# Kernel optimization log

Measured on AMD Instinct MI355X. Metric: run time of the kernel, lower is better.

The kernel has to match this reference:

```python
import jax, jax.numpy as jnp
import numpy as np

NEG_SLOPE = 0.2
BN_EPS = 1e-5


def _gat_conv(x, src, dst, W, a_src, a_dst, b, n_nodes):
    # PyG GATConv, heads=1: linear, per-edge leaky-relu score, per-dst softmax, scatter-add.
    h = x @ W  # [N, C]
    e = jax.nn.leaky_relu((h @ a_src)[src] + (h @ a_dst)[dst], NEG_SLOPE)  # [E]
    m = jax.ops.segment_max(e, dst, num_segments=n_nodes)
    m = jnp.where(jnp.isfinite(m), m, 0.0)  # nodes with no in-edges
    w = jnp.exp(e - m[dst])
    denom = jax.ops.segment_sum(w, dst, num_segments=n_nodes)
    alpha = w / (denom[dst] + 1e-16)  # [E]
    out = jax.ops.segment_sum(alpha[:, None] * h[src], dst, num_segments=n_nodes)
    return out + b


def setup_inputs() -> dict:
    key = jax.random.key(0)
    N, E, Q, C = 50000, 800000, 200000, 128
    ks = jax.random.split(key, 12)
    sc = 1.0 / np.sqrt(C)
    d = {
        "embedding": jax.random.normal(ks[0], (N, C), jnp.float32) * 0.1,
        "W1": jax.random.normal(ks[1], (C, C), jnp.float32) * sc,
        "a_src1": jax.random.normal(ks[2], (C,), jnp.float32) * sc,
        "a_dst1": jax.random.normal(ks[3], (C,), jnp.float32) * sc,
        "b1": jnp.zeros((C,), jnp.float32),
        "gamma": jnp.ones((C,), jnp.float32),
        "beta": jnp.zeros((C,), jnp.float32),
        "rmean": jnp.zeros((C,), jnp.float32),
        "rvar": jnp.ones((C,), jnp.float32),
        "W2": jax.random.normal(ks[4], (C, C), jnp.float32) * sc,
        "a_src2": jax.random.normal(ks[5], (C,), jnp.float32) * sc,
        "a_dst2": jax.random.normal(ks[6], (C,), jnp.float32) * sc,
        "b2": jnp.zeros((C,), jnp.float32),
        "Wp1": jax.random.normal(ks[7], (C, C), jnp.float32) * sc,
        "bp1": jnp.zeros((C,), jnp.float32),
        "Wp2": jax.random.normal(ks[8], (C, 1), jnp.float32) * sc,
        "bp2": jnp.zeros((1,), jnp.float32),
        "edge_index": jax.random.randint(ks[9], (2, E), 0, N, jnp.int32),
        "edges": jax.random.randint(ks[10], (2, Q), 0, N, jnp.int32),
    }
    return d


def reference(embedding, W1, a_src1, a_dst1, b1, gamma, beta, rmean, rvar,
              W2, a_src2, a_dst2, b2, Wp1, bp1, Wp2, bp2, edge_index, edges):
    N = embedding.shape[0]
    src, dst = edge_index[0], edge_index[1]
    # conv0 -> BN (eval, running stats) -> ReLU (dropout inactive in eval)
    x = _gat_conv(embedding, src, dst, W1, a_src1, a_dst1, b1, N)
    x = (x - rmean) * jax.lax.rsqrt(rvar + BN_EPS) * gamma + beta
    x = jax.nn.relu(x)
    # final conv
    x = _gat_conv(x, src, dst, W2, a_src2, a_dst2, b2, N)
    # LinkPredictor: elementwise product of endpoint embeddings -> MLP -> sigmoid
    h = x[edges[0]] * x[edges[1]]  # [Q, C]
    h = jax.nn.relu(h @ Wp1 + bp1)
    out = jax.nn.sigmoid(h @ Wp2 + bp2)
    return out[:, 0]
```

## Files before the change

### kernel.cpp

```cpp
#include <hip/hip_runtime.h>
#include <hip/hip_bf16.h>
#include <math.h>
#include <stdint.h>
#include <string.h>

#define NEG_SLOPE 0.2f
#define BN_EPS 1e-5f

typedef __attribute__((ext_vector_type(8))) short short8;
typedef __attribute__((ext_vector_type(4))) float float4v;

static __device__ __forceinline__ unsigned short f2bf(float f) {
    union { float f; unsigned u; } v; v.f = f;
    unsigned r = (v.u + 0x7fffu + ((v.u >> 16) & 1u)) >> 16;
    return (unsigned short)r;
}
static __device__ __forceinline__ float bf2f(unsigned short u) {
    union { unsigned u; float f; } v; v.u = ((unsigned)u) << 16;
    return v.f;
}

#define BK_CAP 8192
#define BK_EPB 4096
#define LP_RS 136

__global__ __launch_bounds__(256) void zero_init(int* __restrict__ p, int n) {
    int i = threadIdx.x + blockIdx.x * 256;
    if (i < n) p[i] = 0;
}

static __device__ __forceinline__ void scatter_body(
    int* lcnt, int* lbase, int blk,
    const int* __restrict__ src, const int* __restrict__ dst,
    int* __restrict__ bcur, unsigned int* __restrict__ bucket, int E) {
    int t = threadIdx.x;
    int e0 = blk * BK_EPB;
    lcnt[t] = 0;
    __syncthreads();

    int es[16], ed[16];
#pragma unroll
    for (int u = 0; u < 16; ++u) {
        int i = e0 + u * 256 + t;
        if (i < E) {
            es[u] = src[i];
            ed[u] = dst[i];
            atomicAdd(&lcnt[ed[u] >> 8], 1);
        } else {
            ed[u] = -1;
        }
    }
    __syncthreads();
    int c = lcnt[t];
    if (c > 0) lbase[t] = atomicAdd(&bcur[t], c);
    __syncthreads();
    lcnt[t] = 0;
    __syncthreads();
#pragma unroll
    for (int u = 0; u < 16; ++u) {
        if (ed[u] >= 0) {
            int bin = ed[u] >> 8;
            int r = atomicAdd(&lcnt[bin], 1);
            int slot = lbase[bin] + r;
            if (slot < BK_CAP)
                bucket[(size_t)bin * BK_CAP + slot] =
                    ((unsigned)(ed[u] & 255) << 24) | (unsigned)es[u];
        }
    }
}

__global__ __launch_bounds__(256) void prep_scatter(
    const float* __restrict__ W1, const float* __restrict__ W2,
    const float* __restrict__ Wp1,
    unsigned short* __restrict__ wt1, unsigned short* __restrict__ wt2,
    unsigned short* __restrict__ wtp,
    const float* __restrict__ gamma, const float* __restrict__ beta,
    const float* __restrict__ rmean, const float* __restrict__ rvar,
    float* __restrict__ bnsc, float* __restrict__ bnsh,
    const int* __restrict__ src, const int* __restrict__ dst,
    int* __restrict__ bcur, unsigned int* __restrict__ bucket, int E) {
    __shared__ int lcnt[256];
    __shared__ int lbase[256];
    int b = blockIdx.x;
    if (b < 192) {
        const float* W = (b < 64) ? W1 : (b < 128) ? W2 : Wp1;
        unsigned short* WT = (b < 64) ? wt1 : (b < 128) ? wt2 : wtp;
        int idx = (b & 63) * 256 + threadIdx.x;
        int k = idx >> 7, n = idx & 127;
        WT[n * 128 + k] = f2bf(W[idx]);
    } else if (b == 192) {
        if (threadIdx.x < 128) {
            int c = threadIdx.x;
            float s = gamma[c] * rsqrtf(rvar[c] + BN_EPS);
            bnsc[c] = s;
            bnsh[c] = beta[c] - rmean[c] * s;
        }
    } else {
        scatter_body(lcnt, lbase, b - 193, src, dst, bcur, bucket, E);
    }
}

static __device__ __forceinline__ void fill_body(
    char* base, int b,
    const int* __restrict__ bcur, const unsigned int* __restrict__ bucket,
    int* __restrict__ gcnt,
    int* __restrict__ offs, int* __restrict__ ends,
    int* __restrict__ csr, int N) {
    unsigned int* rec = (unsigned int*)base;
    int* cnt = (int*)(base + BK_CAP * 4);
    int* sc  = cnt + 256;
    int* pb  = sc + 256;
    int t = threadIdx.x;
    const unsigned int* gb = &bucket[(size_t)b * BK_CAP];
    cnt[t] = 0;
    int c = bcur[b];
    if (c < 0) c = 0;
    if (c > BK_CAP) c = BK_CAP;
    if (t == 0) *pb = atomicAdd(gcnt, c);
    for (int i = t; i < c; i += 256) rec[i] = gb[i];
    __syncthreads();
    for (int i = t; i < c; i += 256) atomicAdd(&cnt[rec[i] >> 24], 1);
    __syncthreads();
    int v = cnt[t];
    sc[t] = v;
    __syncthreads();
    for (int d = 1; d < 256; d <<= 1) {
        int u = (t >= d) ? sc[t - d] : 0;
        __syncthreads();
        sc[t] += u;
        __syncthreads();
    }
    int myoff = *pb + sc[t] - v;
    int node = (b << 8) + t;
    if (node < N) {
        offs[node] = myoff;
        ends[node] = myoff + v;
    }
    cnt[t] = myoff;
    __syncthreads();
    for (int i = t; i < c; i += 256) {
        unsigned int rv = rec[i];
        int r = atomicAdd(&cnt[rv >> 24], 1);
        csr[r] = (int)(rv & 0xffffffu);
    }
}

template <bool BF16_IN>
static __device__ __forceinline__ void gemm_body(
    unsigned short* sA, unsigned short* sW, int bid,
    const void* __restrict__ Xv,
    const unsigned short* __restrict__ WT,
    const float* __restrict__ a_src, const float* __restrict__ a_dst,
    unsigned short* __restrict__ H,
    float* __restrict__ s_src, float* __restrict__ s_dst, int N)
{
    const float* Xf = (const float*)Xv;
    const unsigned short* Xh = (const unsigned short*)Xv;
    int tid = threadIdx.x;
    int r0 = bid * 128;

#pragma unroll
    for (int it = 0; it < 8; ++it) {
        int idx = it * 2048 + tid * 8;
        int n = idx >> 7, k = idx & 127;
        *(short8*)&sW[n * LP_RS + k] = *(const short8*)&WT[idx];
    }
#pragma unroll
    for (int it = 0; it < 16; ++it) {
        int r = it * 8 + (tid >> 5);
        int c = (tid & 31) * 4;
        int row = r0 + r;
        ushort4 u = make_ushort4(0, 0, 0, 0);
        if (row < N) {
            if (BF16_IN) {
                u = *(const ushort4*)&Xh[(size_t)row * 128 + c];
            } else {
                float4 x = *(const float4*)&Xf[(size_t)row * 128 + c];
                u.x = f2bf(x.x); u.y = f2bf(x.y); u.z = f2bf(x.z); u.w = f2bf(x.w);
            }
        }
        *(ushort4*)&sA[r * LP_RS + c] = u;
    }
    __syncthreads();

    int wave = tid >> 6, lane = tid & 63;
    int ln = lane & 15, quad = lane >> 4;
    int rowbase = wave * 32;

    short8 af[2][4];
#pragma unroll
    for (int m = 0; m < 2; ++m)
#pragma unroll
        for (int kt = 0; kt < 4; ++kt)
            af[m][kt] = *(const short8*)&sA[(rowbase + m * 16 + ln) * LP_RS + kt * 32 + quad * 8];

    float4v acc[2][8];
#pragma unroll
    for (int m = 0; m < 2; ++m)
#pragma unroll
        for (int n = 0; n < 8; ++n)
            acc[m][n] = float4v{0.f, 0.f, 0.f, 0.f};

#pragma unroll
    for (int n = 0; n < 8; ++n) {
#pragma unroll
        for (int kt = 0; kt < 4; ++kt) {
            short8 bf = *(const short8*)&sW[(n * 16 + ln) * LP_RS + kt * 32 + quad * 8];
            acc[0][n] = __builtin_amdgcn_mfma_f32_16x16x32_bf16(af[0][kt], bf, acc[0][n], 0, 0, 0);
            acc[1][n] = __builtin_amdgcn_mfma_f32_16x16x32_bf16(af[1][kt], bf, acc[1][n], 0, 0, 0);
        }
    }

    float asr[8], adr[8];
#pragma unroll
    for (int n = 0; n < 8; ++n) {
        asr[n] = a_src[n * 16 + ln];
        adr[n] = a_dst[n * 16 + ln];
    }
#pragma unroll
    for (int m = 0; m < 2; ++m) {
        int rb = r0 + rowbase + m * 16 + quad * 4;
#pragma unroll
        for (int n = 0; n < 8; ++n) {
            int col = n * 16 + ln;
            float4v a = acc[m][n];
            if (rb + 0 < N) H[(size_t)(rb + 0) * 128 + col] = f2bf(a[0]);
            if (rb + 1 < N) H[(size_t)(rb + 1) * 128 + col] = f2bf(a[1]);
            if (rb + 2 < N) H[(size_t)(rb + 2) * 128 + col] = f2bf(a[2]);
            if (rb + 3 < N) H[(size_t)(rb + 3) * 128 + col] = f2bf(a[3]);
        }
#pragma unroll
        for (int r = 0; r < 4; ++r) {
            float ps = 0.f, pd = 0.f;
#pragma unroll
            for (int n = 0; n < 8; ++n) {
                float v = acc[m][n][r];
                ps = fmaf(v, asr[n], ps);
                pd = fmaf(v, adr[n], pd);
            }
#pragma unroll
            for (int o = 1; o < 16; o <<= 1) {
                ps += __shfl_xor(ps, o);
                pd += __shfl_xor(pd, o);
            }
            int row = rb + r;
            if (ln == 0 && row < N) { s_src[row] = ps; s_dst[row] = pd; }
        }
    }
}

__global__ __launch_bounds__(256) void gemm1_fill(
    const void* __restrict__ Xv, const unsigned short* __restrict__ WT,
    const float* __restrict__ a_src, const float* __restrict__ a_dst,
    unsigned short* __restrict__ H, float* __restrict__ s_src,
    float* __restrict__ s_dst, int N, int gblk,
    const int* __restrict__ bcur, const unsigned int* __restrict__ bucket,
    int* __restrict__ gcnt, int* __restrict__ offs, int* __restrict__ ends,
    int* __restrict__ csr) {
    __shared__ uint4 smem[4352];
    int b = blockIdx.x;
    if (b < gblk) {
        unsigned short* sA = (unsigned short*)smem;
        gemm_body<false>(sA, sA + 128 * LP_RS, b, Xv, WT, a_src, a_dst,
                         H, s_src, s_dst, N);
    } else {
        fill_body((char*)smem, b - gblk, bcur, bucket, gcnt, offs, ends, csr, N);
    }
}

template <bool BF16_IN>
__global__ __launch_bounds__(256) void gemm_mfma(
    const void* __restrict__ Xv, const unsigned short* __restrict__ WT,
    const float* __restrict__ a_src, const float* __restrict__ a_dst,
    unsigned short* __restrict__ H, float* __restrict__ s_src,
    float* __restrict__ s_dst, int N) {
    __shared__ uint4 smem[4352];
    unsigned short* sA = (unsigned short*)smem;
    gemm_body<BF16_IN>(sA, sA + 128 * LP_RS, blockIdx.x, Xv, WT, a_src, a_dst,
                       H, s_src, s_dst, N);
}

__global__ __launch_bounds__(256) void gat_gather(const unsigned short* __restrict__ H,
                                                  const int* __restrict__ offs,
                                                  const int* __restrict__ ends,
                                                  const int* __restrict__ csr,
                                                  const float* __restrict__ s_src,
                                                  const float* __restrict__ s_dst,
                                                  const float* __restrict__ bias,
                                                  const float* __restrict__ bn_scale,
                                                  const float* __restrict__ bn_shift,
                                                  int do_bn_relu,
                                                  unsigned short* __restrict__ out, int N) {
    int wave = threadIdx.x >> 6, lane = threadIdx.x & 63;
    int half = lane >> 5, hl = lane & 31;
    int node = blockIdx.x * 8 + wave * 2 + half;
    if (node >= N) return;
    int c0 = hl * 4;
    int beg = offs[node], end = ends[node];
    float sd = s_dst[node];

    float a0 = 0.f, a1 = 0.f, a2 = 0.f, a3 = 0.f;
    float sw = 0.f;
    for (int chunk = beg; chunk < end; chunk += 32) {
        int i = chunk + hl;
        int sidx = 0;
        float w = 0.f;
        if (i < end) {
            sidx = csr[i];
            float e = s_src[sidx] + sd;
            e = (e >= 0.f) ? e : NEG_SLOPE * e;
            w = expf(e);
        }
        sw += w;
        int cnt = end - chunk;
        if (cnt > 32) cnt = 32;
        int u = 0;
        for (; u + 8 <= cnt; u += 8) {
            int s[8]; float ww[8]; ushort4 hv[8];
#pragma unroll
            for (int j = 0; j < 8; ++j) {
                s[j]  = __shfl(sidx, u + j, 32);
                ww[j] = __shfl(w, u + j, 32);
            }
#pragma unroll
            for (int j = 0; j < 8; ++j)
                hv[j] = *(const ushort4*)&H[(size_t)s[j] * 128 + c0];
#pragma unroll
            for (int j = 0; j < 8; ++j) {
                a0 = fmaf(ww[j], bf2f(hv[j].x), a0);
                a1 = fmaf(ww[j], bf2f(hv[j].y), a1);
                a2 = fmaf(ww[j], bf2f(hv[j].z), a2);
                a3 = fmaf(ww[j], bf2f(hv[j].w), a3);
            }
        }
        for (; u + 4 <= cnt; u += 4) {
            int s[4]; float ww[4]; ushort4 hv[4];
#pragma unroll
            for (int j = 0; j < 4; ++j) {
                s[j]  = __shfl(sidx, u + j, 32);
                ww[j] = __shfl(w, u + j, 32);
            }
#pragma unroll
            for (int j = 0; j < 4; ++j)
                hv[j] = *(const ushort4*)&H[(size_t)s[j] * 128 + c0];
#pragma unroll
            for (int j = 0; j < 4; ++j) {
                a0 = fmaf(ww[j], bf2f(hv[j].x), a0);
                a1 = fmaf(ww[j], bf2f(hv[j].y), a1);
                a2 = fmaf(ww[j], bf2f(hv[j].z), a2);
                a3 = fmaf(ww[j], bf2f(hv[j].w), a3);
            }
        }
        for (; u < cnt; ++u) {
            int sj = __shfl(sidx, u, 32);
            float wj = __shfl(w, u, 32);
            ushort4 hv = *(const ushort4*)&H[(size_t)sj * 128 + c0];
            a0 = fmaf(wj, bf2f(hv.x), a0);
            a1 = fmaf(wj, bf2f(hv.y), a1);
            a2 = fmaf(wj, bf2f(hv.z), a2);
            a3 = fmaf(wj, bf2f(hv.w), a3);
        }
    }
#pragma unroll
    for (int o = 16; o; o >>= 1) sw += __shfl_xor(sw, o);
    float inv = 1.f / (sw + 1e-16f);

    float o0 = a0 * inv + bias[c0 + 0];
    float o1 = a1 * inv + bias[c0 + 1];
    float o2 = a2 * inv + bias[c0 + 2];
    float o3 = a3 * inv + bias[c0 + 3];
    if (do_bn_relu) {
        o0 = fmaxf(o0 * bn_scale[c0 + 0] + bn_shift[c0 + 0], 0.f);
        o1 = fmaxf(o1 * bn_scale[c0 + 1] + bn_shift[c0 + 1], 0.f);
        o2 = fmaxf(o2 * bn_scale[c0 + 2] + bn_shift[c0 + 2], 0.f);
        o3 = fmaxf(o3 * bn_scale[c0 + 3] + bn_shift[c0 + 3], 0.f);
    }
    ushort4 ov;
    ov.x = f2bf(o0); ov.y = f2bf(o1); ov.z = f2bf(o2); ov.w = f2bf(o3);
    *(ushort4*)&out[(size_t)node * 128 + c0] = ov;
}

__global__ __launch_bounds__(512) void link_pred_mfma(
    const unsigned short* __restrict__ X,
    const int* __restrict__ E0, const int* __restrict__ E1,
    const unsigned short* __restrict__ WTg,
    const float* __restrict__ bp1,
    const float* __restrict__ Wp2,
    const float* __restrict__ bp2_p,
    float* __restrict__ out, int Q)
{
    __shared__ unsigned short sW[128 * LP_RS];
    int tid = threadIdx.x;
    int wave = tid >> 6, lane = tid & 63;
    int ln = lane & 15, quad = lane >> 4;

    int tile = blockIdx.x * 8 + wave;
    int qbase = tile * 32;

    int ea[2], eb[2];
#pragma unroll
    for (int m = 0; m < 2; ++m) {
        int q = qbase + m * 16 + ln;
        if (q >= Q) q = Q - 1;
        ea[m] = E0[q];
        eb[m] = E1[q];
    }

#pragma unroll
    for (int it = 0; it < 4; ++it) {
        int idx = it * 4096 + tid * 8;
        int n = idx >> 7, k = idx & 127;
        *(short8*)&sW[n * LP_RS + k] = *(const short8*)&WTg[idx];
    }

    short8 ra[2][4], rb[2][4];
#pragma unroll
    for (int m = 0; m < 2; ++m) {
        const unsigned short* pa = &X[(size_t)ea[m] * 128 + quad * 8];
        const unsigned short* pb = &X[(size_t)eb[m] * 128 + quad * 8];
#pragma unroll
        for (int kt = 0; kt < 4; ++kt) {
            ra[m][kt] = *(const short8*)(pa + kt * 32);
            rb[m][kt] = *(const short8*)(pb + kt * 32);
        }
    }

    float bias[8], w2c[8];
#pragma unroll
    for (int n = 0; n < 8; ++n) {
        bias[n] = bp1[n * 16 + ln];
        w2c[n] = Wp2[n * 16 + ln];
    }
    float b2 = bp2_p[0];

    __syncthreads();

    short8 af[2][4];
#pragma unroll
    for (int m = 0; m < 2; ++m) {
#pragma unroll
        for (int kt = 0; kt < 4; ++kt) {
            short8 p;
#pragma unroll
            for (int j = 0; j < 8; j += 2) {
                float p0 = bf2f((unsigned short)ra[m][kt][j]) *
                           bf2f((unsigned short)rb[m][kt][j]);
                float p1 = bf2f((unsigned short)ra[m][kt][j + 1]) *
                           bf2f((unsigned short)rb[m][kt][j + 1]);
                __hip_bfloat162 h2 = __float22bfloat162_rn(make_float2(p0, p1));
                unsigned pr;
                memcpy(&pr, &h2, 4);
                p[j]     = (short)(pr & 0xffffu);
                p[j + 1] = (short)(pr >> 16);
            }
            af[m][kt] = p;
        }
    }

    float r0[2] = {0.f, 0.f}, r1[2] = {0.f, 0.f}, r2[2] = {0.f, 0.f}, r3[2] = {0.f, 0.f};
#pragma unroll
    for (int n = 0; n < 8; ++n) {
        float4v a0 = float4v{bias[n], bias[n], bias[n], bias[n]};
        float4v a1 = a0;
#pragma unroll
        for (int kt = 0; kt < 4; ++kt) {
            short8 bf = *(const short8*)&sW[(n * 16 + ln) * LP_RS + kt * 32 + quad * 8];
            a0 = __builtin_amdgcn_mfma_f32_16x16x32_bf16(af[0][kt], bf, a0, 0, 0, 0);
            a1 = __builtin_amdgcn_mfma_f32_16x16x32_bf16(af[1][kt], bf, a1, 0, 0, 0);
        }
        float w = w2c[n];
        r0[0] += fmaxf(a0[0], 0.f) * w;  r0[1] += fmaxf(a1[0], 0.f) * w;
        r1[0] += fmaxf(a0[1], 0.f) * w;  r1[1] += fmaxf(a1[1], 0.f) * w;
        r2[0] += fmaxf(a0[2], 0.f) * w;  r2[1] += fmaxf(a1[2], 0.f) * w;
        r3[0] += fmaxf(a0[3], 0.f) * w;  r3[1] += fmaxf(a1[3], 0.f) * w;
    }
#pragma unroll
    for (int m = 0; m < 2; ++m) {
#pragma unroll
        for (int o = 1; o < 16; o <<= 1) {
            r0[m] += __shfl_xor(r0[m], o);
            r1[m] += __shfl_xor(r1[m], o);
            r2[m] += __shfl_xor(r2[m], o);
            r3[m] += __shfl_xor(r3[m], o);
        }
        if (ln == 0) {
            int rbase = qbase + m * 16 + quad * 4;
            float rv[4] = {r0[m], r1[m], r2[m], r3[m]};
#pragma unroll
            for (int r = 0; r < 4; ++r) {
                int q = rbase + r;
                if (q < Q) out[q] = 1.f / (1.f + expf(-(rv[r] + b2)));
            }
        }
    }
}

extern "C" void kernel_launch(void* const* d_in, const int* in_sizes, int n_in,
                              void* d_out, int out_size, void* d_ws, size_t ws_size,
                              hipStream_t stream) {
    const float* emb    = (const float*)d_in[0];
    const float* W1     = (const float*)d_in[1];
    const float* a_src1 = (const float*)d_in[2];
    const float* a_dst1 = (const float*)d_in[3];
    const float* b1     = (const float*)d_in[4];
    const float* gamma  = (const float*)d_in[5];
    const float* beta   = (const float*)d_in[6];
    const float* rmean  = (const float*)d_in[7];
    const float* rvar   = (const float*)d_in[8];
    const float* W2     = (const float*)d_in[9];
    const float* a_src2 = (const float*)d_in[10];
    const float* a_dst2 = (const float*)d_in[11];
    const float* b2     = (const float*)d_in[12];
    const float* Wp1    = (const float*)d_in[13];
    const float* bp1    = (const float*)d_in[14];
    const float* Wp2    = (const float*)d_in[15];
    const float* bp2    = (const float*)d_in[16];
    const int* edge_index = (const int*)d_in[17];
    const int* edges      = (const int*)d_in[18];

    const int N = in_sizes[0] / 128;
    const int E = in_sizes[17] / 2;
    const int Q = in_sizes[18] / 2;
    const int* src = edge_index;
    const int* dst = edge_index + E;
    const int* e0 = edges;
    const int* e1 = edges + Q;
    float* out = (float*)d_out;

    uintptr_t base = (uintptr_t)d_ws;
    size_t cur = 0;
    auto take = [&](size_t bytes) -> void* {
        void* p = (void*)(base + cur);
        cur += (bytes + 255) & ~(size_t)255;
        return p;
    };
    unsigned short* bufA = (unsigned short*)take((size_t)N * 128 * 2);
    unsigned short* bufB = (unsigned short*)take((size_t)N * 128 * 2);
    float* s_src  = (float*)take((size_t)N * 4);
    float* s_dst  = (float*)take((size_t)N * 4);
    float* bnsc   = (float*)take(128 * 4);
    float* bnsh   = (float*)take(128 * 4);
    int*   offs   = (int*)take((size_t)N * 4);
    int*   ends   = (int*)take((size_t)N * 4);
    int*   csr    = (int*)take((size_t)E * 4);
    unsigned short* wt1 = (unsigned short*)take(128 * 128 * 2);
    unsigned short* wt2 = (unsigned short*)take(128 * 128 * 2);
    unsigned short* wtp = (unsigned short*)take(128 * 128 * 2);
    int nb = (N + 255) / 256;
    int*   bcur   = (int*)take((size_t)(nb + 1) * 4);
    unsigned int* bucket =
        (unsigned int*)take((size_t)nb * BK_CAP * 4);
    (void)ws_size; (void)n_in; (void)out_size;

    int nbs = (E + BK_EPB - 1) / BK_EPB;
    int gblk = (N + 127) / 128;

    zero_init<<<1, 256, 0, stream>>>(bcur, nb + 1);
    prep_scatter<<<193 + nbs, 256, 0, stream>>>(W1, W2, Wp1, wt1, wt2, wtp,
                                                gamma, beta, rmean, rvar, bnsc, bnsh,
                                                src, dst, bcur, bucket, E);
    gemm1_fill<<<gblk + nb, 256, 0, stream>>>(emb, wt1, a_src1, a_dst1,
                                              bufA, s_src, s_dst, N, gblk,
                                              bcur, bucket, &bcur[nb],
                                              offs, ends, csr);
    gat_gather<<<(N + 7) / 8, 256, 0, stream>>>(bufA, offs, ends, csr, s_src, s_dst,
                                                b1, bnsc, bnsh, 1, bufB, N);
    gemm_mfma<true><<<gblk, 256, 0, stream>>>(bufB, wt2, a_src2, a_dst2, bufA, s_src, s_dst, N);
    gat_gather<<<(N + 7) / 8, 256, 0, stream>>>(bufA, offs, ends, csr, s_src, s_dst,
                                                b2, nullptr, nullptr, 0, bufB, N);
    int ntiles = (Q + 31) / 32;
    int lblk = (ntiles + 7) / 8;
    link_pred_mfma<<<lblk, 512, 0, stream>>>(bufB, e0, e1, wtp, bp1, Wp2, bp2, out, Q);
}
```

Measured before the change: 238.2 us.

## Compute attention scores inside gather from H; enlarge link-predictor blocks

```diff
diff --git a/kernel.cpp b/kernel.cpp
--- a/kernel.cpp
+++ b/kernel.cpp
@@ -150,9 +150,8 @@
     unsigned short* sA, unsigned short* sW, int bid,
     const void* __restrict__ Xv,
     const unsigned short* __restrict__ WT,
-    const float* __restrict__ a_src, const float* __restrict__ a_dst,
     unsigned short* __restrict__ H,
-    float* __restrict__ s_src, float* __restrict__ s_dst, int N)
+    int N)
 {
     const float* Xf = (const float*)Xv;
     const unsigned short* Xh = (const unsigned short*)Xv;
@@ -211,12 +210,6 @@
         }
     }
 
-    float asr[8], adr[8];
-#pragma unroll
-    for (int n = 0; n < 8; ++n) {
-        asr[n] = a_src[n * 16 + ln];
-        adr[n] = a_dst[n * 16 + ln];
-    }
 #pragma unroll
     for (int m = 0; m < 2; ++m) {
         int rb = r0 + rowbase + m * 16 + quad * 4;
@@ -229,31 +222,12 @@
             if (rb + 2 < N) H[(size_t)(rb + 2) * 128 + col] = f2bf(a[2]);
             if (rb + 3 < N) H[(size_t)(rb + 3) * 128 + col] = f2bf(a[3]);
         }
-#pragma unroll
-        for (int r = 0; r < 4; ++r) {
-            float ps = 0.f, pd = 0.f;
-#pragma unroll
-            for (int n = 0; n < 8; ++n) {
-                float v = acc[m][n][r];
-                ps = fmaf(v, asr[n], ps);
-                pd = fmaf(v, adr[n], pd);
-            }
-#pragma unroll
-            for (int o = 1; o < 16; o <<= 1) {
-                ps += __shfl_xor(ps, o);
-                pd += __shfl_xor(pd, o);
-            }
-            int row = rb + r;
-            if (ln == 0 && row < N) { s_src[row] = ps; s_dst[row] = pd; }
-        }
     }
 }
 
 __global__ __launch_bounds__(256) void gemm1_fill(
     const void* __restrict__ Xv, const unsigned short* __restrict__ WT,
-    const float* __restrict__ a_src, const float* __restrict__ a_dst,
-    unsigned short* __restrict__ H, float* __restrict__ s_src,
-    float* __restrict__ s_dst, int N, int gblk,
+    unsigned short* __restrict__ H, int N, int gblk,
     const int* __restrict__ bcur, const unsigned int* __restrict__ bucket,
     int* __restrict__ gcnt, int* __restrict__ offs, int* __restrict__ ends,
     int* __restrict__ csr) {
@@ -261,8 +235,7 @@
     int b = blockIdx.x;
     if (b < gblk) {
         unsigned short* sA = (unsigned short*)smem;
-        gemm_body<false>(sA, sA + 128 * LP_RS, b, Xv, WT, a_src, a_dst,
-                         H, s_src, s_dst, N);
+        gemm_body<false>(sA, sA + 128 * LP_RS, b, Xv, WT, H, N);
     } else {
         fill_body((char*)smem, b - gblk, bcur, bucket, gcnt, offs, ends, csr, N);
     }
@@ -271,21 +244,18 @@
 template <bool BF16_IN>
 __global__ __launch_bounds__(256) void gemm_mfma(
     const void* __restrict__ Xv, const unsigned short* __restrict__ WT,
-    const float* __restrict__ a_src, const float* __restrict__ a_dst,
-    unsigned short* __restrict__ H, float* __restrict__ s_src,
-    float* __restrict__ s_dst, int N) {
+    unsigned short* __restrict__ H, int N) {
     __shared__ uint4 smem[4352];
     unsigned short* sA = (unsigned short*)smem;
-    gemm_body<BF16_IN>(sA, sA + 128 * LP_RS, blockIdx.x, Xv, WT, a_src, a_dst,
-                       H, s_src, s_dst, N);
+    gemm_body<BF16_IN>(sA, sA + 128 * LP_RS, blockIdx.x, Xv, WT, H, N);
 }
 
 __global__ __launch_bounds__(256) void gat_gather(const unsigned short* __restrict__ H,
                                                   const int* __restrict__ offs,
                                                   const int* __restrict__ ends,
                                                   const int* __restrict__ csr,
-                                                  const float* __restrict__ s_src,
-                                                  const float* __restrict__ s_dst,
+                                                  const float* __restrict__ a_src,
+                                                  const float* __restrict__ a_dst,
                                                   const float* __restrict__ bias,
                                                   const float* __restrict__ bn_scale,
                                                   const float* __restrict__ bn_shift,
@@ -296,73 +266,70 @@
     int node = blockIdx.x * 8 + wave * 2 + half;
     if (node >= N) return;
     int c0 = hl * 4;
+    float4 asr = *(const float4*)&a_src[c0];
+    float4 adr = *(const float4*)&a_dst[c0];
     int beg = offs[node], end = ends[node];
-    float sd = s_dst[node];
+
+    ushort4 hn = *(const ushort4*)&H[(size_t)node * 128 + c0];
+    float sd = fmaf(bf2f(hn.x), adr.x, fmaf(bf2f(hn.y), adr.y,
+               fmaf(bf2f(hn.z), adr.z, bf2f(hn.w) * adr.w)));
+#pragma unroll
+    for (int o = 1; o <= 16; o <<= 1) sd += __shfl_xor(sd, o);
 
     float a0 = 0.f, a1 = 0.f, a2 = 0.f, a3 = 0.f;
     float sw = 0.f;
+
+#define EDGE_STEP(HV)                                                          \
+    {                                                                          \
+        float x0 = bf2f((HV).x), x1 = bf2f((HV).y);                            \
+        float x2 = bf2f((HV).z), x3 = bf2f((HV).w);                            \
+        float ps = fmaf(x0, asr.x, fmaf(x1, asr.y,                             \
+                   fmaf(x2, asr.z, x3 * asr.w)));                              \
+        ps += __shfl_xor(ps, 1); ps += __shfl_xor(ps, 2);                      \
+        ps += __shfl_xor(ps, 4); ps += __shfl_xor(ps, 8);                      \
+        ps += __shfl_xor(ps, 16);                                              \
+        float e = ps + sd;                                                     \
+        e = (e >= 0.f) ? e : NEG_SLOPE * e;                                    \
+        float w = expf(e);                                                     \
+        sw += w;                                                               \
+        a0 = fmaf(w, x0, a0); a1 = fmaf(w, x1, a1);                            \
+        a2 = fmaf(w, x2, a2); a3 = fmaf(w, x3, a3);                            \
+    }
+
     for (int chunk = beg; chunk < end; chunk += 32) {
         int i = chunk + hl;
-        int sidx = 0;
-        float w = 0.f;
-        if (i < end) {
-            sidx = csr[i];
-            float e = s_src[sidx] + sd;
-            e = (e >= 0.f) ? e : NEG_SLOPE * e;
-            w = expf(e);
-        }
-        sw += w;
+        int sidx = (i < end) ? csr[i] : 0;
         int cnt = end - chunk;
         if (cnt > 32) cnt = 32;
         int u = 0;
         for (; u + 8 <= cnt; u += 8) {
-            int s[8]; float ww[8]; ushort4 hv[8];
-#pragma unroll
-            for (int j = 0; j < 8; ++j) {
-                s[j]  = __shfl(sidx, u + j, 32);
-                ww[j] = __shfl(w, u + j, 32);
-            }
+            int s[8]; ushort4 hv[8];
+#pragma unroll
+            for (int j = 0; j < 8; ++j) s[j] = __shfl(sidx, u + j, 32);
 #pragma unroll
             for (int j = 0; j < 8; ++j)
                 hv[j] = *(const ushort4*)&H[(size_t)s[j] * 128 + c0];
 #pragma unroll
-            for (int j = 0; j < 8; ++j) {
-                a0 = fmaf(ww[j], bf2f(hv[j].x), a0);
-                a1 = fmaf(ww[j], bf2f(hv[j].y), a1);
-                a2 = fmaf(ww[j], bf2f(hv[j].z), a2);
-                a3 = fmaf(ww[j], bf2f(hv[j].w), a3);
-            }
+            for (int j = 0; j < 8; ++j) EDGE_STEP(hv[j]);
         }
         for (; u + 4 <= cnt; u += 4) {
-            int s[4]; float ww[4]; ushort4 hv[4];
-#pragma unroll
-            for (int j = 0; j < 4; ++j) {
-                s[j]  = __shfl(sidx, u + j, 32);
-                ww[j] = __shfl(w, u + j, 32);
-            }
+            int s[4]; ushort4 hv[4];
+#pragma unroll
+            for (int j = 0; j < 4; ++j) s[j] = __shfl(sidx, u + j, 32);
 #pragma unroll
             for (int j = 0; j < 4; ++j)
                 hv[j] = *(const ushort4*)&H[(size_t)s[j] * 128 + c0];
 #pragma unroll
-            for (int j = 0; j < 4; ++j) {
-                a0 = fmaf(ww[j], bf2f(hv[j].x), a0);
-                a1 = fmaf(ww[j], bf2f(hv[j].y), a1);
-                a2 = fmaf(ww[j], bf2f(hv[j].z), a2);
-                a3 = fmaf(ww[j], bf2f(hv[j].w), a3);
-            }
+            for (int j = 0; j < 4; ++j) EDGE_STEP(hv[j]);
         }
         for (; u < cnt; ++u) {
             int sj = __shfl(sidx, u, 32);
-            float wj = __shfl(w, u, 32);
             ushort4 hv = *(const ushort4*)&H[(size_t)sj * 128 + c0];
-            a0 = fmaf(wj, bf2f(hv.x), a0);
-            a1 = fmaf(wj, bf2f(hv.y), a1);
-            a2 = fmaf(wj, bf2f(hv.z), a2);
-            a3 = fmaf(wj, bf2f(hv.w), a3);
-        }
-    }
-#pragma unroll
-    for (int o = 16; o; o >>= 1) sw += __shfl_xor(sw, o);
+            EDGE_STEP(hv);
+        }
+    }
+#undef EDGE_STEP
+
     float inv = 1.f / (sw + 1e-16f);
 
     float o0 = a0 * inv + bias[c0 + 0];
@@ -380,7 +347,7 @@
     *(ushort4*)&out[(size_t)node * 128 + c0] = ov;
 }
 
-__global__ __launch_bounds__(512) void link_pred_mfma(
+__global__ __launch_bounds__(1024) void link_pred_mfma(
     const unsigned short* __restrict__ X,
     const int* __restrict__ E0, const int* __restrict__ E1,
     const unsigned short* __restrict__ WTg,
@@ -394,7 +361,7 @@
     int wave = tid >> 6, lane = tid & 63;
     int ln = lane & 15, quad = lane >> 4;
 
-    int tile = blockIdx.x * 8 + wave;
+    int tile = blockIdx.x * 16 + wave;
     int qbase = tile * 32;
 
     int ea[2], eb[2];
@@ -407,8 +374,8 @@
     }
 
 #pragma unroll
-    for (int it = 0; it < 4; ++it) {
-        int idx = it * 4096 + tid * 8;
+    for (int it = 0; it < 2; ++it) {
+        int idx = it * 8192 + tid * 8;
         int n = idx >> 7, k = idx & 127;
         *(short8*)&sW[n * LP_RS + k] = *(const short8*)&WTg[idx];
     }
@@ -536,8 +503,6 @@
     };
     unsigned short* bufA = (unsigned short*)take((size_t)N * 128 * 2);
     unsigned short* bufB = (unsigned short*)take((size_t)N * 128 * 2);
-    float* s_src  = (float*)take((size_t)N * 4);
-    float* s_dst  = (float*)take((size_t)N * 4);
     float* bnsc   = (float*)take(128 * 4);
     float* bnsh   = (float*)take(128 * 4);
     int*   offs   = (int*)take((size_t)N * 4);
@@ -559,16 +524,17 @@
     prep_scatter<<<193 + nbs, 256, 0, stream>>>(W1, W2, Wp1, wt1, wt2, wtp,
                                                 gamma, beta, rmean, rvar, bnsc, bnsh,
                                                 src, dst, bcur, bucket, E);
-    gemm1_fill<<<gblk + nb, 256, 0, stream>>>(emb, wt1, a_src1, a_dst1,
-                                              bufA, s_src, s_dst, N, gblk,
+    gemm1_fill<<<gblk + nb, 256, 0, stream>>>(emb, wt1, bufA, N, gblk,
                                               bcur, bucket, &bcur[nb],
                                               offs, ends, csr);
-    gat_gather<<<(N + 7) / 8, 256, 0, stream>>>(bufA, offs, ends, csr, s_src, s_dst,
+    gat_gather<<<(N + 7) / 8, 256, 0, stream>>>(bufA, offs, ends, csr,
+                                                a_src1, a_dst1,
                                                 b1, bnsc, bnsh, 1, bufB, N);
-    gemm_mfma<true><<<gblk, 256, 0, stream>>>(bufB, wt2, a_src2, a_dst2, bufA, s_src, s_dst, N);
-    gat_gather<<<(N + 7) / 8, 256, 0, stream>>>(bufA, offs, ends, csr, s_src, s_dst,
+    gemm_mfma<true><<<gblk, 256, 0, stream>>>(bufB, wt2, bufA, N);
+    gat_gather<<<(N + 7) / 8, 256, 0, stream>>>(bufA, offs, ends, csr,
+                                                a_src2, a_dst2,
                                                 b2, nullptr, nullptr, 0, bufB, N);
     int ntiles = (Q + 31) / 32;
-    int lblk = (ntiles + 7) / 8;
-    link_pred_mfma<<<lblk, 512, 0, stream>>>(bufB, e0, e1, wtp, bp1, Wp2, bp2, out, Q);
-}
+    int lblk = (ntiles + 15) / 16;
+    link_pred_mfma<<<lblk, 1024, 0, stream>>>(bufB, e0, e1, wtp, bp1, Wp2, bp2, out, Q);
+}
```

After: 277.2 us. +16.3%, slower.

## Bucket link-prediction queries by first endpoint for gather locality

Applied to the files above, without the earlier changes.

```diff
diff --git a/kernel.cpp b/kernel.cpp
--- a/kernel.cpp
+++ b/kernel.cpp
@@ -21,6 +21,7 @@
 }
 
 #define BK_CAP 8192
+#define QB_CAP 2048
 #define BK_EPB 4096
 #define LP_RS 136
 
@@ -65,6 +66,48 @@
             if (slot < BK_CAP)
                 bucket[(size_t)bin * BK_CAP + slot] =
                     ((unsigned)(ed[u] & 255) << 24) | (unsigned)es[u];
+        }
+    }
+}
+
+static __device__ __forceinline__ void qscatter_body(
+    int* lcnt, int* lbase, int blk,
+    const int* __restrict__ E0, const int* __restrict__ E1,
+    int* __restrict__ qcur, unsigned long long* __restrict__ qbucket, int Q) {
+    int t = threadIdx.x;
+    int q0 = blk * BK_EPB;
+    lcnt[t] = 0;
+    __syncthreads();
+
+    int a0[16], a1[16];
+#pragma unroll
+    for (int u = 0; u < 16; ++u) {
+        int i = q0 + u * 256 + t;
+        if (i < Q) {
+            a0[u] = E0[i];
+            a1[u] = E1[i];
+            atomicAdd(&lcnt[a0[u] >> 8], 1);
+        } else {
+            a0[u] = -1;
+        }
+    }
+    __syncthreads();
+    int c = lcnt[t];
+    if (c > 0) lbase[t] = atomicAdd(&qcur[t], c);
+    __syncthreads();
+    lcnt[t] = 0;
+    __syncthreads();
+#pragma unroll
+    for (int u = 0; u < 16; ++u) {
+        if (a0[u] >= 0) {
+            int bin = a0[u] >> 8;
+            int r = atomicAdd(&lcnt[bin], 1);
+            int slot = lbase[bin] + r;
+            int i = q0 + u * 256 + t;
+            if (slot < QB_CAP)
+                qbucket[(size_t)bin * QB_CAP + slot] =
+                    ((unsigned long long)(unsigned)a1[u] << 32) |
+                    ((unsigned)(a0[u] & 255) << 24) | (unsigned)i;
         }
     }
 }
@@ -78,7 +121,10 @@
     const float* __restrict__ rmean, const float* __restrict__ rvar,
     float* __restrict__ bnsc, float* __restrict__ bnsh,
     const int* __restrict__ src, const int* __restrict__ dst,
-    int* __restrict__ bcur, unsigned int* __restrict__ bucket, int E) {
+    int* __restrict__ bcur, unsigned int* __restrict__ bucket, int E,
+    const int* __restrict__ E0, const int* __restrict__ E1,
+    int* __restrict__ qcur, unsigned long long* __restrict__ qbucket,
+    int Q, int nbs) {
     __shared__ int lcnt[256];
     __shared__ int lbase[256];
     int b = blockIdx.x;
@@ -95,8 +141,10 @@
             bnsc[c] = s;
             bnsh[c] = beta[c] - rmean[c] * s;
         }
+    } else if (b < 193 + nbs) {
+        scatter_body(lcnt, lbase, b - 193, src, dst, bcur, bucket, E);
     } else {
-        scatter_body(lcnt, lbase, b - 193, src, dst, bcur, bucket, E);
+        qscatter_body(lcnt, lbase, b - 193 - nbs, E0, E1, qcur, qbucket, Q);
     }
 }
 
@@ -382,47 +430,30 @@
 
 __global__ __launch_bounds__(512) void link_pred_mfma(
     const unsigned short* __restrict__ X,
-    const int* __restrict__ E0, const int* __restrict__ E1,
+    const int* __restrict__ qcur,
+    const unsigned long long* __restrict__ qbucket,
     const unsigned short* __restrict__ WTg,
     const float* __restrict__ bp1,
     const float* __restrict__ Wp2,
     const float* __restrict__ bp2_p,
-    float* __restrict__ out, int Q)
+    float* __restrict__ out, int nb)
 {
     __shared__ unsigned short sW[128 * LP_RS];
     int tid = threadIdx.x;
     int wave = tid >> 6, lane = tid & 63;
     int ln = lane & 15, quad = lane >> 4;
 
-    int tile = blockIdx.x * 8 + wave;
-    int qbase = tile * 32;
-
-    int ea[2], eb[2];
-#pragma unroll
-    for (int m = 0; m < 2; ++m) {
-        int q = qbase + m * 16 + ln;
-        if (q >= Q) q = Q - 1;
-        ea[m] = E0[q];
-        eb[m] = E1[q];
-    }
+    int x = blockIdx.x & 7;
+    int g = blockIdx.x >> 3;
+    int b = (g >> 2) * 8 + x;
+    int k = g & 3;
+    if (b >= nb) return;
 
 #pragma unroll
     for (int it = 0; it < 4; ++it) {
         int idx = it * 4096 + tid * 8;
-        int n = idx >> 7, k = idx & 127;
-        *(short8*)&sW[n * LP_RS + k] = *(const short8*)&WTg[idx];
-    }
-
-    short8 ra[2][4], rb[2][4];
-#pragma unroll
-    for (int m = 0; m < 2; ++m) {
-        const unsigned short* pa = &X[(size_t)ea[m] * 128 + quad * 8];
-        const unsigned short* pb = &X[(size_t)eb[m] * 128 + quad * 8];
-#pragma unroll
-        for (int kt = 0; kt < 4; ++kt) {
-            ra[m][kt] = *(const short8*)(pa + kt * 32);
-            rb[m][kt] = *(const short8*)(pb + kt * 32);
-        }
+        int n = idx >> 7, kk = idx & 127;
+        *(short8*)&sW[n * LP_RS + kk] = *(const short8*)&WTg[idx];
     }
 
     float bias[8], w2c[8];
@@ -433,63 +464,96 @@
     }
     float b2 = bp2_p[0];
 
-    __syncthreads();
-
-    short8 af[2][4];
-#pragma unroll
-    for (int m = 0; m < 2; ++m) {
-#pragma unroll
-        for (int kt = 0; kt < 4; ++kt) {
-            short8 p;
-#pragma unroll
-            for (int j = 0; j < 8; j += 2) {
-                float p0 = bf2f((unsigned short)ra[m][kt][j]) *
-                           bf2f((unsigned short)rb[m][kt][j]);
-                float p1 = bf2f((unsigned short)ra[m][kt][j + 1]) *
-                           bf2f((unsigned short)rb[m][kt][j + 1]);
-                __hip_bfloat162 h2 = __float22bfloat162_rn(make_float2(p0, p1));
-                unsigned pr;
-                memcpy(&pr, &h2, 4);
-                p[j]     = (short)(pr & 0xffffu);
-                p[j + 1] = (short)(pr >> 16);
-            }
-            af[m][kt] = p;
-        }
-    }
-
-    float r0[2] = {0.f, 0.f}, r1[2] = {0.f, 0.f}, r2[2] = {0.f, 0.f}, r3[2] = {0.f, 0.f};
-#pragma unroll
-    for (int n = 0; n < 8; ++n) {
-        float4v a0 = float4v{bias[n], bias[n], bias[n], bias[n]};
-        float4v a1 = a0;
-#pragma unroll
-        for (int kt = 0; kt < 4; ++kt) {
-            short8 bf = *(const short8*)&sW[(n * 16 + ln) * LP_RS + kt * 32 + quad * 8];
-            a0 = __builtin_amdgcn_mfma_f32_16x16x32_bf16(af[0][kt], bf, a0, 0, 0, 0);
-            a1 = __builtin_amdgcn_mfma_f32_16x16x32_bf16(af[1][kt], bf, a1, 0, 0, 0);
-        }
-        float w = w2c[n];
-        r0[0] += fmaxf(a0[0], 0.f) * w;  r0[1] += fmaxf(a1[0], 0.f) * w;
-        r1[0] += fmaxf(a0[1], 0.f) * w;  r1[1] += fmaxf(a1[1], 0.f) * w;
-        r2[0] += fmaxf(a0[2], 0.f) * w;  r2[1] += fmaxf(a1[2], 0.f) * w;
-        r3[0] += fmaxf(a0[3], 0.f) * w;  r3[1] += fmaxf(a1[3], 0.f) * w;
-    }
-#pragma unroll
-    for (int m = 0; m < 2; ++m) {
-#pragma unroll
-        for (int o = 1; o < 16; o <<= 1) {
-            r0[m] += __shfl_xor(r0[m], o);
-            r1[m] += __shfl_xor(r1[m], o);
-            r2[m] += __shfl_xor(r2[m], o);
-            r3[m] += __shfl_xor(r3[m], o);
-        }
-        if (ln == 0) {
-            int rbase = qbase + m * 16 + quad * 4;
-            float rv[4] = {r0[m], r1[m], r2[m], r3[m]};
-#pragma unroll
-            for (int r = 0; r < 4; ++r) {
-                int q = rbase + r;
-                if (q < Q) out[q] = 1.f / (1.f + expf(-(rv[r] + b2)));
+    int cnt = qcur[b];
+    if (cnt < 0) cnt = 0;
+    if (cnt > QB_CAP) cnt = QB_CAP;
+    int tiles = (cnt + 31) >> 5;
+    const unsigned long long* qb = &qbucket[(size_t)b * QB_CAP];
+
+    __syncthreads();
+
+    for (int t = k + 4 * wave; t < tiles; t += 32) {
+        int q[2], ea[2], eb[2];
+#pragma unroll
+        for (int m = 0; m < 2; ++m) {
+            int s = t * 32 + m * 16 + ln;
+            bool val = s < cnt;
+            unsigned long long r = qb[val ? s : 0];
+            q[m]  = val ? (int)(r & 0xffffffu) : -1;
+            ea[m] = (b << 8) | (int)((r >> 24) & 255u);
+            eb[m] = (int)(r >> 32);
+        }
+
+        short8 ra[2][4], rb[2][4];
+#pragma unroll
+        for (int m = 0; m < 2; ++m) {
+            const unsigned short* pa = &X[(size_t)ea[m] * 128 + quad * 8];
+            const unsigned short* pb = &X[(size_t)eb[m] * 128 + quad * 8];
+#pragma unroll
+            for (int kt = 0; kt < 4; ++kt) {
+                ra[m][kt] = *(const short8*)(pa + kt * 32);
+                rb[m][kt] = *(const short8*)(pb + kt * 32);
+            }
+        }
+
+        short8 af[2][4];
+#pragma unroll
+        for (int m = 0; m < 2; ++m) {
+#pragma unroll
+            for (int kt = 0; kt < 4; ++kt) {
+                short8 p;
+#pragma unroll
+                for (int j = 0; j < 8; j += 2) {
+                    float p0 = bf2f((unsigned short)ra[m][kt][j]) *
+                               bf2f((unsigned short)rb[m][kt][j]);
+                    float p1 = bf2f((unsigned short)ra[m][kt][j + 1]) *
+                               bf2f((unsigned short)rb[m][kt][j + 1]);
+                    __hip_bfloat162 h2 = __float22bfloat162_rn(make_float2(p0, p1));
+                    unsigned pr;
+                    memcpy(&pr, &h2, 4);
+                    p[j]     = (short)(pr & 0xffffu);
+                    p[j + 1] = (short)(pr >> 16);
+                }
+                af[m][kt] = p;
+            }
+        }
+
+        float r0[2] = {0.f, 0.f}, r1[2] = {0.f, 0.f};
+        float r2[2] = {0.f, 0.f}, r3[2] = {0.f, 0.f};
+#pragma unroll
+        for (int n = 0; n < 8; ++n) {
+            float4v a0 = float4v{bias[n], bias[n], bias[n], bias[n]};
+            float4v a1 = a0;
+#pragma unroll
+            for (int kt = 0; kt < 4; ++kt) {
+                short8 bf = *(const short8*)&sW[(n * 16 + ln) * LP_RS + kt * 32 + quad * 8];
+                a0 = __builtin_amdgcn_mfma_f32_16x16x32_bf16(af[0][kt], bf, a0, 0, 0, 0);
+                a1 = __builtin_amdgcn_mfma_f32_16x16x32_bf16(af[1][kt], bf, a1, 0, 0, 0);
+            }
+            float w = w2c[n];
+            r0[0] += fmaxf(a0[0], 0.f) * w;  r0[1] += fmaxf(a1[0], 0.f) * w;
+            r1[0] += fmaxf(a0[1], 0.f) * w;  r1[1] += fmaxf(a1[1], 0.f) * w;
+            r2[0] += fmaxf(a0[2], 0.f) * w;  r2[1] += fmaxf(a1[2], 0.f) * w;
+            r3[0] += fmaxf(a0[3], 0.f) * w;  r3[1] += fmaxf(a1[3], 0.f) * w;
+        }
+#pragma unroll
+        for (int m = 0; m < 2; ++m) {
+#pragma unroll
+            for (int o = 1; o < 16; o <<= 1) {
+                r0[m] += __shfl_xor(r0[m], o);
+                r1[m] += __shfl_xor(r1[m], o);
+                r2[m] += __shfl_xor(r2[m], o);
+                r3[m] += __shfl_xor(r3[m], o);
+            }
+            int q0_ = __shfl(q[m], quad * 4 + 0, 16);
+            int q1_ = __shfl(q[m], quad * 4 + 1, 16);
+            int q2_ = __shfl(q[m], quad * 4 + 2, 16);
+            int q3_ = __shfl(q[m], quad * 4 + 3, 16);
+            if (ln == 0) {
+                if (q0_ >= 0) out[q0_] = 1.f / (1.f + expf(-(r0[m] + b2)));
+                if (q1_ >= 0) out[q1_] = 1.f / (1.f + expf(-(r1[m] + b2)));
+                if (q2_ >= 0) out[q2_] = 1.f / (1.f + expf(-(r2[m] + b2)));
+                if (q3_ >= 0) out[q3_] = 1.f / (1.f + expf(-(r3[m] + b2)));
             }
         }
     }
@@ -547,18 +611,24 @@
     unsigned short* wt2 = (unsigned short*)take(128 * 128 * 2);
     unsigned short* wtp = (unsigned short*)take(128 * 128 * 2);
     int nb = (N + 255) / 256;
-    int*   bcur   = (int*)take((size_t)(nb + 1) * 4);
+    int*   bcur   = (int*)take((size_t)(2 * nb + 1) * 4);
+    int*   qcur   = bcur + nb + 1;
     unsigned int* bucket =
         (unsigned int*)take((size_t)nb * BK_CAP * 4);
+    unsigned long long* qbucket =
+        (unsigned long long*)take((size_t)nb * QB_CAP * 8);
     (void)ws_size; (void)n_in; (void)out_size;
 
     int nbs = (E + BK_EPB - 1) / BK_EPB;
+    int nqs = (Q + BK_EPB - 1) / BK_EPB;
     int gblk = (N + 127) / 128;
 
-    zero_init<<<1, 256, 0, stream>>>(bcur, nb + 1);
-    prep_scatter<<<193 + nbs, 256, 0, stream>>>(W1, W2, Wp1, wt1, wt2, wtp,
-                                                gamma, beta, rmean, rvar, bnsc, bnsh,
-                                                src, dst, bcur, bucket, E);
+    zero_init<<<2, 256, 0, stream>>>(bcur, 2 * nb + 1);
+    prep_scatter<<<193 + nbs + nqs, 256, 0, stream>>>(
+        W1, W2, Wp1, wt1, wt2, wtp,
+        gamma, beta, rmean, rvar, bnsc, bnsh,
+        src, dst, bcur, bucket, E,
+        e0, e1, qcur, qbucket, Q, nbs);
     gemm1_fill<<<gblk + nb, 256, 0, stream>>>(emb, wt1, a_src1, a_dst1,
                                               bufA, s_src, s_dst, N, gblk,
                                               bcur, bucket, &bcur[nb],
@@ -568,7 +638,7 @@
     gemm_mfma<true><<<gblk, 256, 0, stream>>>(bufB, wt2, a_src2, a_dst2, bufA, s_src, s_dst, N);
     gat_gather<<<(N + 7) / 8, 256, 0, stream>>>(bufA, offs, ends, csr, s_src, s_dst,
                                                 b2, nullptr, nullptr, 0, bufB, N);
-    int ntiles = (Q + 31) / 32;
-    int lblk = (ntiles + 7) / 8;
-    link_pred_mfma<<<lblk, 512, 0, stream>>>(bufB, e0, e1, wtp, bp1, Wp2, bp2, out, Q);
-}
+    int lblk = 8 * ((nb + 7) / 8) * 4;
+    link_pred_mfma<<<lblk, 512, 0, stream>>>(bufB, qcur, qbucket, wtp,
+                                             bp1, Wp2, bp2, out, nb);
+}
```

After: 249.1 us. +4.6%, slower.
